# Kernel tuning notes

Hardware: AMD Instinct MI355X
Metric: run time of the kernel (lower is better)

The kernel has to match this reference:

```python
import jax, jax.numpy as jnp
import numpy as np

N_NODES = 100000
SELF_LOOP_W = 2.0  # improved=True in PyG GCNConv -> self-loop fill value 2.0


def gcn_conv(x, src, dst, ew, W, b, n_nodes):
    """PyG GCNConv (improved=True): x' = D^-1/2 (A + 2I) D^-1/2 (x W) + b."""
    h = x @ W  # [N, out]
    loop = jnp.arange(n_nodes, dtype=src.dtype)
    src_f = jnp.concatenate([src, loop])
    dst_f = jnp.concatenate([dst, loop])
    ew_f = jnp.concatenate([ew, jnp.full((n_nodes,), SELF_LOOP_W, dtype=ew.dtype)])
    deg = jax.ops.segment_sum(ew_f, dst_f, num_segments=n_nodes)  # [N]
    dinv = jnp.where(deg > 0, jax.lax.rsqrt(jnp.where(deg > 0, deg, 1.0)), 0.0)
    norm = dinv[src_f] * ew_f * dinv[dst_f]  # [E+N]
    msg = h[src_f] * norm[:, None]  # [E+N, out]
    out = jax.ops.segment_sum(msg, dst_f, num_segments=n_nodes)
    return out + b


def setup_inputs() -> dict:
    key = jax.random.key(0)
    k1, k2, k3, k4, k5 = jax.random.split(key, 5)
    N, E = N_NODES, 3200000
    F0, F1, F2 = 128, 128, 64
    x = jax.random.normal(k1, (N, F0), dtype=jnp.float32)
    edges = jax.random.randint(k2, (2, E), 0, N, dtype=jnp.int64)
    weights = jax.random.uniform(k3, (E,), dtype=jnp.float32)
    # kaiming_uniform on weight of shape [out, in]; stored transposed for x @ W
    bnd0 = float(np.sqrt(6.0 / F0))
    bnd1 = float(np.sqrt(6.0 / F1))
    W0 = jax.random.uniform(k4, (F0, F1), dtype=jnp.float32, minval=-bnd0, maxval=bnd0)
    W1 = jax.random.uniform(k5, (F1, F2), dtype=jnp.float32, minval=-bnd1, maxval=bnd1)
    b0 = jnp.zeros((F1,), dtype=jnp.float32)
    b1 = jnp.zeros((F2,), dtype=jnp.float32)
    return {"x": x, "edges": edges, "weights": weights,
            "W0": W0, "b0": b0, "W1": W1, "b1": b1}


def reference(x, edges, weights, W0, b0, W1, b1):
    src, dst = edges[0], edges[1]
    n = x.shape[0]
    h = gcn_conv(x, src, dst, weights, W0, b0, n)
    h = jax.nn.relu(h)
    h = gcn_conv(h, src, dst, weights, W1, b1, n)
    return jax.nn.sigmoid(h)
```

## Files before the change

kernel.cpp:

```cpp
#include <hip/hip_runtime.h>
#include <math.h>

typedef __attribute__((ext_vector_type(8))) short bf16x8;
typedef __attribute__((ext_vector_type(4))) float f32x4;


__device__ __forceinline__ unsigned short f2b(float f) {
  unsigned u = __float_as_uint(f);
  unsigned r = u + 0x7fffu + ((u >> 16) & 1u);
  return (unsigned short)(r >> 16);
}
__device__ __forceinline__ float b2f_lo(unsigned v) {
  return __uint_as_float(v << 16);
}
__device__ __forceinline__ float b2f_hi(unsigned v) {
  return __uint_as_float(v & 0xffff0000u);
}


__global__ __launch_bounds__(256) void bucket_hist(const int* __restrict__ dst,
                                                   int* __restrict__ blkhist,
                                                   int NB, int E, int chunk) {
  extern __shared__ int sm_hist[];
  for (int i = threadIdx.x; i < NB; i += 256) sm_hist[i] = 0;
  __syncthreads();
  const int b = blockIdx.x;
  const int beg = b * chunk;
  const int end = min(E, beg + chunk);
  for (int j = beg + threadIdx.x; j < end; j += 256)
    atomicAdd(&sm_hist[dst[j] >> 6], 1);
  __syncthreads();
  for (int i = threadIdx.x; i < NB; i += 256) blkhist[(long)b * NB + i] = sm_hist[i];
}

__global__ __launch_bounds__(256) void col_prefix(int* __restrict__ blkhist,
                                                  int* __restrict__ btot, int NB,
                                                  int nblk) {
  const int k = blockIdx.x * 256 + threadIdx.x;
  if (k >= NB) return;
  int run = 0;
  int b = 0;
  for (; b + 4 <= nblk; b += 4) {
    const int t0 = blkhist[(long)(b + 0) * NB + k];
    const int t1 = blkhist[(long)(b + 1) * NB + k];
    const int t2 = blkhist[(long)(b + 2) * NB + k];
    const int t3 = blkhist[(long)(b + 3) * NB + k];
    blkhist[(long)(b + 0) * NB + k] = run; run += t0;
    blkhist[(long)(b + 1) * NB + k] = run; run += t1;
    blkhist[(long)(b + 2) * NB + k] = run; run += t2;
    blkhist[(long)(b + 3) * NB + k] = run; run += t3;
  }
  for (; b < nblk; ++b) {
    const int t = blkhist[(long)b * NB + k];
    blkhist[(long)b * NB + k] = run;
    run += t;
  }
  btot[k] = run;
}

__global__ __launch_bounds__(256) void scan_single(int* __restrict__ cr, int n) {
  __shared__ int sm[256];
  __shared__ int sbase;
  if (threadIdx.x == 0) sbase = 0;
  __syncthreads();
  for (int c0 = 0; c0 < n; c0 += 256) {
    const int i = c0 + threadIdx.x;
    const int v = (i < n) ? cr[i] : 0;
    sm[threadIdx.x] = v;
    __syncthreads();
    for (int off = 1; off < 256; off <<= 1) {
      int a = (threadIdx.x >= off) ? sm[threadIdx.x - off] : 0;
      __syncthreads();
      sm[threadIdx.x] += a;
      __syncthreads();
    }
    const int b = sbase;
    const int tot = sm[255];
    if (i < n) cr[i] = b + sm[threadIdx.x] - v;
    __syncthreads();
    if (threadIdx.x == 0) sbase = b + tot;
    __syncthreads();
  }
  if (threadIdx.x == 0) cr[n] = sbase;
}

__global__ __launch_bounds__(256) void bucket_scatter(const int* __restrict__ src,
                                                      const int* __restrict__ dst,
                                                      const float* __restrict__ ew,
                                                      const int* __restrict__ blkhist,
                                                      const int* __restrict__ bstart,
                                                      uint2* __restrict__ bkt, int NB,
                                                      int E, int chunk) {
  extern __shared__ int sm_cur[];
  const int b = blockIdx.x;
  for (int i = threadIdx.x; i < NB; i += 256)
    sm_cur[i] = blkhist[(long)b * NB + i] + bstart[i];
  __syncthreads();
  const int beg = b * chunk;
  const int end = min(E, beg + chunk);
  for (int j = beg + threadIdx.x; j < end; j += 256) {
    const int d = dst[j];
    int q = (int)(ew[j] * 32767.f + 0.5f);
    q = (q < 0) ? 0 : ((q > 32767) ? 32767 : q);
    const unsigned rec = ((unsigned)src[j] << 15) | (unsigned)q;
    const int pos = atomicAdd(&sm_cur[d >> 6], 1);
    bkt[pos] = make_uint2(rec, (unsigned)(d & 63));
  }
}

__global__ __launch_bounds__(256) void bucket_finalize(const uint2* __restrict__ bkt,
                                                       const int* __restrict__ bstart,
                                                       unsigned* __restrict__ recs,
                                                       int* __restrict__ row_start,
                                                       float* __restrict__ dinv, int NB,
                                                       int N, int E) {
  __shared__ int hist[64], qs[64], cur[64], lstart[64];
  const int k = blockIdx.x;
  const int t = threadIdx.x;
  if (t < 64) { hist[t] = 0; qs[t] = 0; }
  __syncthreads();
  const int beg = bstart[k], end = bstart[k + 1];
  for (int j = beg + t; j < end; j += 256) {
    const uint2 v = bkt[j];
    atomicAdd(&hist[v.y], 1);
    atomicAdd(&qs[v.y], (int)(v.x & 32767u));
  }
  __syncthreads();
  if (t == 0) {
    int run = 0;
    for (int i = 0; i < 64; ++i) { lstart[i] = run; run += hist[i]; }
  }
  __syncthreads();
  if (t < 64) {
    cur[t] = lstart[t];
    const int node = k * 64 + t;
    if (node < N) {
      row_start[node] = beg + lstart[t];
      dinv[node] = rsqrtf((float)qs[t] * (1.f / 32767.f) + 2.0f);
    }
  }
  if (k == NB - 1 && t == 0) row_start[N] = E;
  __syncthreads();
  for (int j = beg + t; j < end; j += 256) {
    const uint2 v = bkt[j];
    const int off = atomicAdd(&cur[v.y], 1);
    recs[beg + off] = v.x;
  }
}


__global__ __launch_bounds__(256) void fold_dinv(unsigned int* __restrict__ recs,
                                                 const float* __restrict__ dinv, int E) {
  int i = blockIdx.x * 256 + threadIdx.x;
  if (i >= E) return;
  const unsigned rec = recs[i];
  const int s = rec >> 15;
  const float v = (float)(rec & 32767u) * (1.f / 32767.f) * dinv[s];
  int q = (int)(v * (32767.f / 0.75f) + 0.5f);
  q = (q > 32767) ? 32767 : q;
  recs[i] = ((unsigned)s << 15) | (unsigned)q;
}


__global__ __launch_bounds__(256) void to_bf16_8(const float* __restrict__ x,
                                                 unsigned short* __restrict__ xb,
                                                 int n8) {
  int i = blockIdx.x * 256 + threadIdx.x;
  if (i >= n8) return;
  const float4 a = *(const float4*)&x[(long)i * 8];
  const float4 b = *(const float4*)&x[(long)i * 8 + 4];
  uint4 o;
  o.x = (unsigned)f2b(a.x) | ((unsigned)f2b(a.y) << 16);
  o.y = (unsigned)f2b(a.z) | ((unsigned)f2b(a.w) << 16);
  o.z = (unsigned)f2b(b.x) | ((unsigned)f2b(b.y) << 16);
  o.w = (unsigned)f2b(b.z) | ((unsigned)f2b(b.w) << 16);
  *(uint4*)&xb[(long)i * 8] = o;
}

__global__ __launch_bounds__(256) void pack_wfrag(const float* __restrict__ W,
                                                  unsigned short* __restrict__ frag,
                                                  int C, int total) {
  int i = blockIdx.x * 256 + threadIdx.x;
  if (i >= total) return;
  const int e = i & 7;
  const int lane = (i >> 3) & 63;
  const int t = i >> 9;
  const int kk = t & 3;
  const int ct = t >> 2;
  const int k = kk * 32 + (lane >> 4) * 8 + e;
  const int c = ct * 16 + (lane & 15);
  frag[i] = f2b(W[(long)k * C + c]);
}


__global__ __launch_bounds__(256) void gather_l1_half(const uint4* __restrict__ xb4,
                                                      const unsigned int* __restrict__ recs,
                                                      const int* __restrict__ row_start,
                                                      const float* __restrict__ dinv,
                                                      uint4* __restrict__ xab4, int N,
                                                      int half) {
  const int t = blockIdx.x * 256 + threadIdx.x;
  const int d = t >> 3;
  if (d >= N) return;
  const int jl = (t & 7) + half * 8;
  const int beg = row_start[d], end = row_start[d + 1];
  const float dd = dinv[d];
  constexpr float S = 0.75f / 32767.f;
  const uint4 sv = xb4[(long)d * 16 + jl];
  const float sl = 2.f * dd * dd;
  float aca[8], acb[8];
  aca[0] = b2f_lo(sv.x) * sl; aca[1] = b2f_hi(sv.x) * sl;
  aca[2] = b2f_lo(sv.y) * sl; aca[3] = b2f_hi(sv.y) * sl;
  aca[4] = b2f_lo(sv.z) * sl; aca[5] = b2f_hi(sv.z) * sl;
  aca[6] = b2f_lo(sv.w) * sl; aca[7] = b2f_hi(sv.w) * sl;
#pragma unroll
  for (int u = 0; u < 8; ++u) acb[u] = 0.f;
  int j = beg;
  for (; j + 8 <= end; j += 8) {
    unsigned rr[8];
    uint4 vv[8];
#pragma unroll
    for (int u = 0; u < 8; ++u) rr[u] = recs[j + u];
#pragma unroll
    for (int u = 0; u < 8; ++u) vv[u] = xb4[(long)(rr[u] >> 15) * 16 + jl];
#pragma unroll
    for (int u = 0; u < 8; ++u) {
      const float cf = (float)(rr[u] & 32767u) * S * dd;
      float* ac = (u & 1) ? acb : aca;
      ac[0] = fmaf(cf, b2f_lo(vv[u].x), ac[0]);
      ac[1] = fmaf(cf, b2f_hi(vv[u].x), ac[1]);
      ac[2] = fmaf(cf, b2f_lo(vv[u].y), ac[2]);
      ac[3] = fmaf(cf, b2f_hi(vv[u].y), ac[3]);
      ac[4] = fmaf(cf, b2f_lo(vv[u].z), ac[4]);
      ac[5] = fmaf(cf, b2f_hi(vv[u].z), ac[5]);
      ac[6] = fmaf(cf, b2f_lo(vv[u].w), ac[6]);
      ac[7] = fmaf(cf, b2f_hi(vv[u].w), ac[7]);
    }
  }
  for (; j < end; ++j) {
    const unsigned rec = recs[j];
    const uint4 v = xb4[(long)(rec >> 15) * 16 + jl];
    const float cf = (float)(rec & 32767u) * S * dd;
    aca[0] = fmaf(cf, b2f_lo(v.x), aca[0]);
    aca[1] = fmaf(cf, b2f_hi(v.x), aca[1]);
    aca[2] = fmaf(cf, b2f_lo(v.y), aca[2]);
    aca[3] = fmaf(cf, b2f_hi(v.y), aca[3]);
    aca[4] = fmaf(cf, b2f_lo(v.z), aca[4]);
    aca[5] = fmaf(cf, b2f_hi(v.z), aca[5]);
    aca[6] = fmaf(cf, b2f_lo(v.w), aca[6]);
    aca[7] = fmaf(cf, b2f_hi(v.w), aca[7]);
  }
#pragma unroll
  for (int u = 0; u < 8; ++u) aca[u] += acb[u];
  uint4 o;
  o.x = (unsigned)f2b(aca[0]) | ((unsigned)f2b(aca[1]) << 16);
  o.y = (unsigned)f2b(aca[2]) | ((unsigned)f2b(aca[3]) << 16);
  o.z = (unsigned)f2b(aca[4]) | ((unsigned)f2b(aca[5]) << 16);
  o.w = (unsigned)f2b(aca[6]) | ((unsigned)f2b(aca[7]) << 16);
  xab4[(long)d * 16 + jl] = o;
}


__global__ __launch_bounds__(256) void fused_mlp_mfma(
    const unsigned short* __restrict__ xab, const unsigned short* __restrict__ w0f,
    const float* __restrict__ b0, const unsigned short* __restrict__ w1f,
    unsigned short* __restrict__ r2b, int N) {
  __shared__ unsigned short Hl[4][16][136];
  const int tid = threadIdx.x;
  const int w = tid >> 6, l = tid & 63;
  const int lr = l & 15, lg = l >> 4;
  const int row0 = blockIdx.x * 64 + w * 16;

  int arow = row0 + lr;
  if (arow >= N) arow = N - 1;
  const unsigned short* ap = xab + (long)arow * 128 + lg * 8;
  const bf16x8 a0 = *(const bf16x8*)(ap);
  const bf16x8 a1 = *(const bf16x8*)(ap + 32);
  const bf16x8 a2 = *(const bf16x8*)(ap + 64);
  const bf16x8 a3 = *(const bf16x8*)(ap + 96);

  for (int ct = 0; ct < 8; ++ct) {
    const unsigned short* bp = w0f + ct * 2048 + l * 8;
    f32x4 acc = {0.f, 0.f, 0.f, 0.f};
    acc = __builtin_amdgcn_mfma_f32_16x16x32_bf16(a0, *(const bf16x8*)(bp), acc, 0, 0, 0);
    acc = __builtin_amdgcn_mfma_f32_16x16x32_bf16(a1, *(const bf16x8*)(bp + 512), acc, 0, 0, 0);
    acc = __builtin_amdgcn_mfma_f32_16x16x32_bf16(a2, *(const bf16x8*)(bp + 1024), acc, 0, 0, 0);
    acc = __builtin_amdgcn_mfma_f32_16x16x32_bf16(a3, *(const bf16x8*)(bp + 1536), acc, 0, 0, 0);
    const float bv = b0[ct * 16 + lr];
#pragma unroll
    for (int r = 0; r < 4; ++r) {
      Hl[w][lg * 4 + r][ct * 16 + lr] = f2b(fmaxf(acc[r] + bv, 0.f));
    }
  }

  const unsigned short* hp = &Hl[w][lr][lg * 8];
  const bf16x8 h0 = *(const bf16x8*)(hp);
  const bf16x8 h1 = *(const bf16x8*)(hp + 32);
  const bf16x8 h2 = *(const bf16x8*)(hp + 64);
  const bf16x8 h3 = *(const bf16x8*)(hp + 96);

  for (int ct = 0; ct < 4; ++ct) {
    const unsigned short* bp = w1f + ct * 2048 + l * 8;
    f32x4 acc = {0.f, 0.f, 0.f, 0.f};
    acc = __builtin_amdgcn_mfma_f32_16x16x32_bf16(h0, *(const bf16x8*)(bp), acc, 0, 0, 0);
    acc = __builtin_amdgcn_mfma_f32_16x16x32_bf16(h1, *(const bf16x8*)(bp + 512), acc, 0, 0, 0);
    acc = __builtin_amdgcn_mfma_f32_16x16x32_bf16(h2, *(const bf16x8*)(bp + 1024), acc, 0, 0, 0);
    acc = __builtin_amdgcn_mfma_f32_16x16x32_bf16(h3, *(const bf16x8*)(bp + 1536), acc, 0, 0, 0);
#pragma unroll
    for (int r = 0; r < 4; ++r) {
      const int orow = row0 + lg * 4 + r;
      if (orow < N) r2b[(long)orow * 64 + ct * 16 + lr] = f2b(acc[r]);
    }
  }
}


__global__ __launch_bounds__(256) void gather_l2(const uint4* __restrict__ r2b4,
                                                 const unsigned int* __restrict__ recs,
                                                 const int* __restrict__ row_start,
                                                 const float* __restrict__ dinv,
                                                 const float* __restrict__ b1,
                                                 float* __restrict__ out, int N) {
  const int t = blockIdx.x * 256 + threadIdx.x;
  const int d = t >> 3;
  if (d >= N) return;
  const int jl = t & 7;
  const int beg = row_start[d], end = row_start[d + 1];
  const float dd = dinv[d];
  constexpr float S = 0.75f / 32767.f;
  const uint4 sv = r2b4[(long)d * 8 + jl];
  const float sl = 2.f * dd * dd;
  float aca[8], acb[8];
  aca[0] = b2f_lo(sv.x) * sl; aca[1] = b2f_hi(sv.x) * sl;
  aca[2] = b2f_lo(sv.y) * sl; aca[3] = b2f_hi(sv.y) * sl;
  aca[4] = b2f_lo(sv.z) * sl; aca[5] = b2f_hi(sv.z) * sl;
  aca[6] = b2f_lo(sv.w) * sl; aca[7] = b2f_hi(sv.w) * sl;
#pragma unroll
  for (int u = 0; u < 8; ++u) acb[u] = 0.f;
  int j = beg;
  for (; j + 8 <= end; j += 8) {
    unsigned rr[8];
    uint4 vv[8];
#pragma unroll
    for (int u = 0; u < 8; ++u) rr[u] = recs[j + u];
#pragma unroll
    for (int u = 0; u < 8; ++u) vv[u] = r2b4[(long)(rr[u] >> 15) * 8 + jl];
#pragma unroll
    for (int u = 0; u < 8; ++u) {
      const float cf = (float)(rr[u] & 32767u) * S * dd;
      float* ac = (u & 1) ? acb : aca;
      ac[0] = fmaf(cf, b2f_lo(vv[u].x), ac[0]);
      ac[1] = fmaf(cf, b2f_hi(vv[u].x), ac[1]);
      ac[2] = fmaf(cf, b2f_lo(vv[u].y), ac[2]);
      ac[3] = fmaf(cf, b2f_hi(vv[u].y), ac[3]);
      ac[4] = fmaf(cf, b2f_lo(vv[u].z), ac[4]);
      ac[5] = fmaf(cf, b2f_hi(vv[u].z), ac[5]);
      ac[6] = fmaf(cf, b2f_lo(vv[u].w), ac[6]);
      ac[7] = fmaf(cf, b2f_hi(vv[u].w), ac[7]);
    }
  }
  for (; j < end; ++j) {
    const unsigned rec = recs[j];
    const uint4 v = r2b4[(long)(rec >> 15) * 8 + jl];
    const float cf = (float)(rec & 32767u) * S * dd;
    aca[0] = fmaf(cf, b2f_lo(v.x), aca[0]);
    aca[1] = fmaf(cf, b2f_hi(v.x), aca[1]);
    aca[2] = fmaf(cf, b2f_lo(v.y), aca[2]);
    aca[3] = fmaf(cf, b2f_hi(v.y), aca[3]);
    aca[4] = fmaf(cf, b2f_lo(v.z), aca[4]);
    aca[5] = fmaf(cf, b2f_hi(v.z), aca[5]);
    aca[6] = fmaf(cf, b2f_lo(v.w), aca[6]);
    aca[7] = fmaf(cf, b2f_hi(v.w), aca[7]);
  }
#pragma unroll
  for (int u = 0; u < 8; ++u) aca[u] += acb[u];
  const int c = jl * 8;
  const float4 ba = *(const float4*)&b1[c];
  const float4 bb = *(const float4*)&b1[c + 4];
  float4 o1, o2;
  o1.x = 1.f / (1.f + __expf(-(aca[0] + ba.x)));
  o1.y = 1.f / (1.f + __expf(-(aca[1] + ba.y)));
  o1.z = 1.f / (1.f + __expf(-(aca[2] + ba.z)));
  o1.w = 1.f / (1.f + __expf(-(aca[3] + ba.w)));
  o2.x = 1.f / (1.f + __expf(-(aca[4] + bb.x)));
  o2.y = 1.f / (1.f + __expf(-(aca[5] + bb.y)));
  o2.z = 1.f / (1.f + __expf(-(aca[6] + bb.z)));
  o2.w = 1.f / (1.f + __expf(-(aca[7] + bb.w)));
  *(float4*)&out[(long)d * 64 + c] = o1;
  *(float4*)&out[(long)d * 64 + c + 4] = o2;
}


extern "C" void kernel_launch(void* const* d_in, const int* in_sizes, int n_in,
                              void* d_out, int out_size, void* d_ws, size_t ws_size,
                              hipStream_t stream) {
  const float* x  = (const float*)d_in[0];
  const int* src  = (const int*)d_in[1];
  const float* ew = (const float*)d_in[2];
  const float* W0 = (const float*)d_in[3];
  const float* b0 = (const float*)d_in[4];
  const float* W1 = (const float*)d_in[5];
  const float* b1 = (const float*)d_in[6];
  float* out = (float*)d_out;

  const int N = in_sizes[0] / 128;
  const int E = in_sizes[2];
  const int* dstp = src + E;

  const int NB = (N + 63) >> 6;
  const int NBLK = 256;
  const int chunk = (E + NBLK - 1) / NBLK;

  float* ws = (float*)d_ws;
  const size_t oN = ((size_t)N + 255) & ~(size_t)255;
  float* dinv = ws;
  int* rowst = (int*)(ws + oN);
  int* bstart = rowst + oN;
  int* bsum = bstart + 2048;
  int* blkhist = bsum + 1024;
  unsigned int* recs = (unsigned int*)(blkhist + (size_t)NBLK * NB);
  unsigned int* xb = recs + E;
  uint2* bkt = (uint2*)xb;
  const size_t xb_units = ((size_t)2 * E > (size_t)N * 64) ? (size_t)2 * E : (size_t)N * 64;
  unsigned int* xab = xb + xb_units;
  unsigned short* w0f = (unsigned short*)(xab + (size_t)N * 64);
  unsigned short* w1f = w0f + 16384;
  unsigned int* r2b = xb;

  const int nbE = (E + 255) / 256;
  const int nblkB = (NB + 255) / 256;

  bucket_hist<<<NBLK, 256, NB * 4, stream>>>(dstp, blkhist, NB, E, chunk);
  col_prefix<<<nblkB, 256, 0, stream>>>(blkhist, bstart, NB, NBLK);
  scan_single<<<1, 256, 0, stream>>>(bstart, NB);
  bucket_scatter<<<NBLK, 256, NB * 4, stream>>>(src, dstp, ew, blkhist, bstart, bkt, NB,
                                                E, chunk);
  bucket_finalize<<<NB, 256, 0, stream>>>(bkt, bstart, recs, rowst, dinv, NB, N, E);
  fold_dinv<<<nbE, 256, 0, stream>>>(recs, dinv, E);

  pack_wfrag<<<64, 256, 0, stream>>>(W0, w0f, 128, 16384);
  pack_wfrag<<<32, 256, 0, stream>>>(W1, w1f, 64, 8192);
  to_bf16_8<<<(N * 16 + 255) / 256, 256, 0, stream>>>(x, (unsigned short*)xb, N * 16);

  const int gl1b = (N * 8 + 255) / 256;
  gather_l1_half<<<gl1b, 256, 0, stream>>>((const uint4*)xb, recs, rowst, dinv,
                                           (uint4*)xab, N, 0);
  gather_l1_half<<<gl1b, 256, 0, stream>>>((const uint4*)xb, recs, rowst, dinv,
                                           (uint4*)xab, N, 1);

  fused_mlp_mfma<<<(N + 63) / 64, 256, 0, stream>>>((const unsigned short*)xab, w0f, b0,
                                                    w1f, (unsigned short*)r2b, N);
  gather_l2<<<(N * 8 + 255) / 256, 256, 0, stream>>>((const uint4*)r2b, recs, rowst, dinv,
                                                     b1, out, N);
}
```

Measured before the change: 328.8 us.

## Fuse bucket histogram and scatter into one pass with fixed-capacity slabs

```diff
diff --git a/kernel.cpp b/kernel.cpp
--- a/kernel.cpp
+++ b/kernel.cpp
@@ -3,6 +3,8 @@
 
 typedef __attribute__((ext_vector_type(8))) short bf16x8;
 typedef __attribute__((ext_vector_type(4))) float f32x4;
+
+#define NBLK 1024
 
 
 __device__ __forceinline__ unsigned short f2b(float f) {
@@ -18,44 +20,9 @@
 }
 
 
-__global__ __launch_bounds__(256) void bucket_hist(const int* __restrict__ dst,
-                                                   int* __restrict__ blkhist,
-                                                   int NB, int E, int chunk) {
-  extern __shared__ int sm_hist[];
-  for (int i = threadIdx.x; i < NB; i += 256) sm_hist[i] = 0;
-  __syncthreads();
-  const int b = blockIdx.x;
-  const int beg = b * chunk;
-  const int end = min(E, beg + chunk);
-  for (int j = beg + threadIdx.x; j < end; j += 256)
-    atomicAdd(&sm_hist[dst[j] >> 6], 1);
-  __syncthreads();
-  for (int i = threadIdx.x; i < NB; i += 256) blkhist[(long)b * NB + i] = sm_hist[i];
-}
-
-__global__ __launch_bounds__(256) void col_prefix(int* __restrict__ blkhist,
-                                                  int* __restrict__ btot, int NB,
-                                                  int nblk) {
-  const int k = blockIdx.x * 256 + threadIdx.x;
-  if (k >= NB) return;
-  int run = 0;
-  int b = 0;
-  for (; b + 4 <= nblk; b += 4) {
-    const int t0 = blkhist[(long)(b + 0) * NB + k];
-    const int t1 = blkhist[(long)(b + 1) * NB + k];
-    const int t2 = blkhist[(long)(b + 2) * NB + k];
-    const int t3 = blkhist[(long)(b + 3) * NB + k];
-    blkhist[(long)(b + 0) * NB + k] = run; run += t0;
-    blkhist[(long)(b + 1) * NB + k] = run; run += t1;
-    blkhist[(long)(b + 2) * NB + k] = run; run += t2;
-    blkhist[(long)(b + 3) * NB + k] = run; run += t3;
-  }
-  for (; b < nblk; ++b) {
-    const int t = blkhist[(long)b * NB + k];
-    blkhist[(long)b * NB + k] = run;
-    run += t;
-  }
-  btot[k] = run;
+__global__ __launch_bounds__(256) void zero_i32(int* __restrict__ p, int n) {
+  int i = blockIdx.x * 256 + threadIdx.x;
+  if (i < n) p[i] = 0;
 }
 
 __global__ __launch_bounds__(256) void scan_single(int* __restrict__ cr, int n) {
@@ -84,65 +51,105 @@
   if (threadIdx.x == 0) cr[n] = sbase;
 }
 
-__global__ __launch_bounds__(256) void bucket_scatter(const int* __restrict__ src,
-                                                      const int* __restrict__ dst,
-                                                      const float* __restrict__ ew,
-                                                      const int* __restrict__ blkhist,
-                                                      const int* __restrict__ bstart,
-                                                      uint2* __restrict__ bkt, int NB,
-                                                      int E, int chunk) {
-  extern __shared__ int sm_cur[];
+
+__global__ __launch_bounds__(256) void scatter_fused(const int* __restrict__ src,
+                                                     const int* __restrict__ dst,
+                                                     const float* __restrict__ ew,
+                                                     int* __restrict__ gcur,
+                                                     uint2* __restrict__ bkt, int NB,
+                                                     int cap, int E, int chunk) {
+  extern __shared__ int hist[];
   const int b = blockIdx.x;
-  for (int i = threadIdx.x; i < NB; i += 256)
-    sm_cur[i] = blkhist[(long)b * NB + i] + bstart[i];
+  for (int i = threadIdx.x; i < NB; i += 256) hist[i] = 0;
   __syncthreads();
   const int beg = b * chunk;
   const int end = min(E, beg + chunk);
-  for (int j = beg + threadIdx.x; j < end; j += 256) {
+  int j = beg + threadIdx.x;
+  for (; j + 768 < end; j += 1024) {
+    const int d0 = dst[j], d1 = dst[j + 256], d2 = dst[j + 512], d3 = dst[j + 768];
+    atomicAdd(&hist[d0 >> 8], 1);
+    atomicAdd(&hist[d1 >> 8], 1);
+    atomicAdd(&hist[d2 >> 8], 1);
+    atomicAdd(&hist[d3 >> 8], 1);
+  }
+  for (; j < end; j += 256) atomicAdd(&hist[dst[j] >> 8], 1);
+  __syncthreads();
+  for (int i = threadIdx.x; i < NB; i += 256) {
+    const int c = hist[i];
+    hist[i] = (c > 0) ? atomicAdd(&gcur[i], c) : 0;
+  }
+  __syncthreads();
+  j = beg + threadIdx.x;
+  for (; j + 768 < end; j += 1024) {
+    const int d0 = dst[j], d1 = dst[j + 256], d2 = dst[j + 512], d3 = dst[j + 768];
+    const int s0 = src[j], s1 = src[j + 256], s2 = src[j + 512], s3 = src[j + 768];
+    const float e0 = ew[j], e1 = ew[j + 256], e2 = ew[j + 512], e3 = ew[j + 768];
+    int q0 = (int)(e0 * 32767.f + 0.5f); q0 = (q0 < 0) ? 0 : ((q0 > 32767) ? 32767 : q0);
+    int q1 = (int)(e1 * 32767.f + 0.5f); q1 = (q1 < 0) ? 0 : ((q1 > 32767) ? 32767 : q1);
+    int q2 = (int)(e2 * 32767.f + 0.5f); q2 = (q2 < 0) ? 0 : ((q2 > 32767) ? 32767 : q2);
+    int q3 = (int)(e3 * 32767.f + 0.5f); q3 = (q3 < 0) ? 0 : ((q3 > 32767) ? 32767 : q3);
+    const int k0 = d0 >> 8, k1 = d1 >> 8, k2 = d2 >> 8, k3 = d3 >> 8;
+    const int p0 = atomicAdd(&hist[k0], 1);
+    if (p0 < cap) bkt[(long)k0 * cap + p0] =
+        make_uint2(((unsigned)s0 << 15) | (unsigned)q0, (unsigned)(d0 & 255));
+    const int p1 = atomicAdd(&hist[k1], 1);
+    if (p1 < cap) bkt[(long)k1 * cap + p1] =
+        make_uint2(((unsigned)s1 << 15) | (unsigned)q1, (unsigned)(d1 & 255));
+    const int p2 = atomicAdd(&hist[k2], 1);
+    if (p2 < cap) bkt[(long)k2 * cap + p2] =
+        make_uint2(((unsigned)s2 << 15) | (unsigned)q2, (unsigned)(d2 & 255));
+    const int p3 = atomicAdd(&hist[k3], 1);
+    if (p3 < cap) bkt[(long)k3 * cap + p3] =
+        make_uint2(((unsigned)s3 << 15) | (unsigned)q3, (unsigned)(d3 & 255));
+  }
+  for (; j < end; j += 256) {
     const int d = dst[j];
     int q = (int)(ew[j] * 32767.f + 0.5f);
     q = (q < 0) ? 0 : ((q > 32767) ? 32767 : q);
     const unsigned rec = ((unsigned)src[j] << 15) | (unsigned)q;
-    const int pos = atomicAdd(&sm_cur[d >> 6], 1);
-    bkt[pos] = make_uint2(rec, (unsigned)(d & 63));
+    const int k = d >> 8;
+    const int pos = atomicAdd(&hist[k], 1);
+    if (pos < cap) bkt[(long)k * cap + pos] = make_uint2(rec, (unsigned)(d & 255));
   }
 }
 
 __global__ __launch_bounds__(256) void bucket_finalize(const uint2* __restrict__ bkt,
                                                        const int* __restrict__ bstart,
+                                                       int cap,
                                                        unsigned* __restrict__ recs,
                                                        int* __restrict__ row_start,
                                                        float* __restrict__ dinv, int NB,
                                                        int N, int E) {
-  __shared__ int hist[64], qs[64], cur[64], lstart[64];
+  __shared__ int hist[256], qs[256], cur[256], lstart[256];
   const int k = blockIdx.x;
   const int t = threadIdx.x;
-  if (t < 64) { hist[t] = 0; qs[t] = 0; }
-  __syncthreads();
-  const int beg = bstart[k], end = bstart[k + 1];
-  for (int j = beg + t; j < end; j += 256) {
-    const uint2 v = bkt[j];
+  hist[t] = 0;
+  qs[t] = 0;
+  __syncthreads();
+  const int beg = bstart[k];
+  const int cnt = bstart[k + 1] - beg;
+  const uint2* slab = bkt + (long)k * cap;
+  for (int j = t; j < cnt; j += 256) {
+    const uint2 v = slab[j];
     atomicAdd(&hist[v.y], 1);
     atomicAdd(&qs[v.y], (int)(v.x & 32767u));
   }
   __syncthreads();
   if (t == 0) {
     int run = 0;
-    for (int i = 0; i < 64; ++i) { lstart[i] = run; run += hist[i]; }
-  }
-  __syncthreads();
-  if (t < 64) {
-    cur[t] = lstart[t];
-    const int node = k * 64 + t;
-    if (node < N) {
-      row_start[node] = beg + lstart[t];
-      dinv[node] = rsqrtf((float)qs[t] * (1.f / 32767.f) + 2.0f);
-    }
+    for (int i = 0; i < 256; ++i) { lstart[i] = run; run += hist[i]; }
+  }
+  __syncthreads();
+  cur[t] = lstart[t];
+  const int node = k * 256 + t;
+  if (node < N) {
+    row_start[node] = beg + lstart[t];
+    dinv[node] = rsqrtf((float)qs[t] * (1.f / 32767.f) + 2.0f);
   }
   if (k == NB - 1 && t == 0) row_start[N] = E;
   __syncthreads();
-  for (int j = beg + t; j < end; j += 256) {
-    const uint2 v = bkt[j];
+  for (int j = t; j < cnt; j += 256) {
+    const uint2 v = slab[j];
     const int off = atomicAdd(&cur[v.y], 1);
     recs[beg + off] = v.x;
   }
@@ -407,8 +414,8 @@
   const int E = in_sizes[2];
   const int* dstp = src + E;
 
-  const int NB = (N + 63) >> 6;
-  const int NBLK = 256;
+  const int NB = (N + 255) >> 8;
+  const int cap = E / NB + 1024;
   const int chunk = (E + NBLK - 1) / NBLK;
 
   float* ws = (float*)d_ws;
@@ -416,26 +423,23 @@
   float* dinv = ws;
   int* rowst = (int*)(ws + oN);
   int* bstart = rowst + oN;
-  int* bsum = bstart + 2048;
-  int* blkhist = bsum + 1024;
-  unsigned int* recs = (unsigned int*)(blkhist + (size_t)NBLK * NB);
+  unsigned int* recs = (unsigned int*)(bstart + 2048);
   unsigned int* xb = recs + E;
   uint2* bkt = (uint2*)xb;
-  const size_t xb_units = ((size_t)2 * E > (size_t)N * 64) ? (size_t)2 * E : (size_t)N * 64;
+  const size_t bkt_units = (size_t)2 * NB * cap;
+  const size_t xb_units = (bkt_units > (size_t)N * 64) ? bkt_units : (size_t)N * 64;
   unsigned int* xab = xb + xb_units;
   unsigned short* w0f = (unsigned short*)(xab + (size_t)N * 64);
   unsigned short* w1f = w0f + 16384;
   unsigned int* r2b = xb;
 
   const int nbE = (E + 255) / 256;
-  const int nblkB = (NB + 255) / 256;
-
-  bucket_hist<<<NBLK, 256, NB * 4, stream>>>(dstp, blkhist, NB, E, chunk);
-  col_prefix<<<nblkB, 256, 0, stream>>>(blkhist, bstart, NB, NBLK);
+
+  zero_i32<<<8, 256, 0, stream>>>(bstart, 2048);
+  scatter_fused<<<NBLK, 256, NB * 4, stream>>>(src, dstp, ew, bstart, bkt, NB, cap, E,
+                                               chunk);
   scan_single<<<1, 256, 0, stream>>>(bstart, NB);
-  bucket_scatter<<<NBLK, 256, NB * 4, stream>>>(src, dstp, ew, blkhist, bstart, bkt, NB,
-                                                E, chunk);
-  bucket_finalize<<<NB, 256, 0, stream>>>(bkt, bstart, recs, rowst, dinv, NB, N, E);
+  bucket_finalize<<<NB, 256, 0, stream>>>(bkt, bstart, cap, recs, rowst, dinv, NB, N, E);
   fold_dinv<<<nbE, 256, 0, stream>>>(recs, dinv, E);
 
   pack_wfrag<<<64, 256, 0, stream>>>(W0, w0f, 128, 16384);
```

Result: no change. 326.2 us (-0.8%).
